# Optimization experiments

Measured on AMD Instinct MI355X. Metric: run time of the kernel, lower is better.

Reference implementation:

```python
import jax, jax.numpy as jnp
import numpy as np

EMBED_DIM = 512
HEADS = 8
ATTN_DIM = EMBED_DIM // HEADS
PF_DIM = 2048
B, L = 4, 2048
LN_EPS = 1e-5


def _linear(x, W, b):
    # nn.Linear: x @ W.T + b, W is [out, in]
    return jnp.einsum('bld,od->blo', x, W) + b


def _layer_norm(x, g, b):
    mu = jnp.mean(x, axis=-1, keepdims=True)
    var = jnp.mean(jnp.square(x - mu), axis=-1, keepdims=True)
    return (x - mu) * jax.lax.rsqrt(var + LN_EPS) * g + b


def _qkv(src, Wq, bq, Wk, bk, Wv, bv):
    def split(t):
        Bb, Ll, _ = t.shape
        return t.reshape(Bb, Ll, HEADS, ATTN_DIM).transpose(0, 2, 1, 3)  # [B,H,L,Dh]
    return (split(_linear(src, Wq, bq)),
            split(_linear(src, Wk, bk)),
            split(_linear(src, Wv, bv)))


def _attention(inp, Q, K1, K2, V1, V2, Wo, bo, ln_g, ln_b, W1, b1, W2, b2):
    # non-softmax linear attention: (Q K1^T) V1 + (Q K2^T) V2
    attn = (jnp.einsum('bhqk,bhkd->bhqd', jnp.einsum('bhqd,bhkd->bhqk', Q, K1), V1)
            + jnp.einsum('bhqk,bhkd->bhqd', jnp.einsum('bhqd,bhkd->bhqk', Q, K2), V2))
    Bb = Q.shape[0]
    attn = attn.transpose(0, 2, 1, 3).reshape(Bb, -1, HEADS * ATTN_DIM)  # [B,L,D]
    x = _linear(attn, Wo, bo)
    x = _layer_norm(inp + x, ln_g, ln_b)          # dropout p=0 (eval)
    ff = _linear(jax.nn.relu(_linear(x, W1, b1)), W2, b2)
    x = _layer_norm(x + ff, ln_g, ln_b)
    return x


def setup_inputs() -> dict:
    key = jax.random.key(0)
    ks = jax.random.split(key, 16)
    s = 0.02
    return {
        'question': jax.random.normal(ks[0], (B, L, EMBED_DIM), jnp.float32),
        'query': jax.random.normal(ks[1], (B, L, EMBED_DIM), jnp.float32),
        'Wq': jax.random.normal(ks[2], (EMBED_DIM, EMBED_DIM), jnp.float32) * s,
        'bq': jnp.zeros((EMBED_DIM,), jnp.float32),
        'Wk': jax.random.normal(ks[3], (EMBED_DIM, EMBED_DIM), jnp.float32) * s,
        'bk': jnp.zeros((EMBED_DIM,), jnp.float32),
        'Wv': jax.random.normal(ks[4], (EMBED_DIM, EMBED_DIM), jnp.float32) * s,
        'bv': jnp.zeros((EMBED_DIM,), jnp.float32),
        'Wo': jax.random.normal(ks[5], (EMBED_DIM, EMBED_DIM), jnp.float32) * s,
        'bo': jnp.zeros((EMBED_DIM,), jnp.float32),
        'ln_g': jnp.ones((EMBED_DIM,), jnp.float32),
        'ln_b': jnp.zeros((EMBED_DIM,), jnp.float32),
        'W1': jax.random.normal(ks[6], (PF_DIM, EMBED_DIM), jnp.float32) * s,
        'b1': jnp.zeros((PF_DIM,), jnp.float32),
        'W2': jax.random.normal(ks[7], (EMBED_DIM, PF_DIM), jnp.float32) * s,
        'b2': jnp.zeros((EMBED_DIM,), jnp.float32),
    }


def reference(question, query, Wq, bq, Wk, bk, Wv, bv, Wo, bo, ln_g, ln_b, W1, b1, W2, b2):
    Q1, K1, V1 = _qkv(question, Wq, bq, Wk, bk, Wv, bv)
    Q2, K2, V2 = _qkv(query, Wq, bq, Wk, bk, Wv, bv)
    question_attn = _attention(question, Q1, K1, K2, V1, V2, Wo, bo, ln_g, ln_b, W1, b1, W2, b2)
    query_attn = _attention(query, Q2, K2, K1, V2, V1, Wo, bo, ln_g, ln_b, W1, b1, W2, b2)
    return jnp.concatenate([question_attn, query_attn], axis=-1)
```

## Files before the change

### kernel.cpp

```cpp
#include <hip/hip_runtime.h>
#include <stdint.h>


#define Bq 4
#define Lq 2048
#define Dq 512
#define PFq 2048
#define Mrows 16384
#define MiBu 1048576ull

typedef __attribute__((ext_vector_type(8))) short frag_ab;
typedef __attribute__((ext_vector_type(4))) float frag_cd;
typedef __attribute__((ext_vector_type(8))) unsigned short ushort8v;

__device__ __forceinline__ unsigned short f2b(float f) {
    union { float f; uint32_t u; } x; x.f = f;
    uint32_t r = x.u + 0x7fffu + ((x.u >> 16) & 1u);
    return (unsigned short)(r >> 16);
}
__device__ __forceinline__ float b2f(unsigned short u) {
    union { uint32_t u; float f; } x; x.u = ((uint32_t)u) << 16;
    return x.f;
}

#define GLD16(g, l)                                                              \
    __builtin_amdgcn_global_load_lds(                                            \
        (const __attribute__((address_space(1))) void*)(const void*)(g),         \
        (__attribute__((address_space(3))) void*)(void*)(l), 16, 0, 0)

__global__ __launch_bounds__(256) void gemm_bf16(
    const unsigned short* __restrict__ A, const unsigned short* __restrict__ Wt,
    const float* __restrict__ bias, unsigned short* __restrict__ outB,
    int M, int N, int K, int relu)
{
    __shared__ __align__(16) unsigned short Sh[2 * 128 * 64];
    unsigned short* At = Sh;
    unsigned short* Bt = Sh + 128 * 64;
    const int tid = threadIdx.x;
    const int lane = tid & 63;
    const int w = tid >> 6;
    const int wm = (w >> 1) * 64, wn = (w & 1) * 64;
    const int lr = lane & 15;
    const int quad = lane >> 4;
    const size_t bm = (size_t)blockIdx.x * 128, bn = (size_t)blockIdx.y * 128;

    frag_cd acc[4][4] = {};

    const int ar = tid >> 3;
    const int acs = (((tid & 7) ^ (ar & 7)) << 3);
    const unsigned short* Ag = A  + (bm + ar) * (size_t)K + acs;
    const unsigned short* Bg = Wt + (bn + ar) * (size_t)K + acs;
    unsigned short* Asd = At + w * 512;
    unsigned short* Bsd = Bt + w * 512;

    for (int k0 = 0; k0 < K; k0 += 64) {
        __syncthreads();
#pragma unroll
        for (int i = 0; i < 4; ++i) {
            GLD16(Ag + (size_t)(32 * i) * K + k0, Asd + i * 2048);
            GLD16(Bg + (size_t)(32 * i) * K + k0, Bsd + i * 2048);
        }
        __syncthreads();
#pragma unroll
        for (int kk = 0; kk < 2; ++kk) {
            frag_ab a[4], b[4];
#pragma unroll
            for (int i = 0; i < 4; ++i)
                a[i] = *(const frag_ab*)&At[(wm + i * 16 + lr) * 64 +
                                            ((((kk << 2) | quad) ^ (lr & 7)) << 3)];
#pragma unroll
            for (int j = 0; j < 4; ++j)
                b[j] = *(const frag_ab*)&Bt[(wn + j * 16 + lr) * 64 +
                                            ((((kk << 2) | quad) ^ (lr & 7)) << 3)];
#pragma unroll
            for (int i = 0; i < 4; ++i)
#pragma unroll
                for (int j = 0; j < 4; ++j)
                    acc[i][j] = __builtin_amdgcn_mfma_f32_16x16x32_bf16(a[i], b[j], acc[i][j], 0, 0, 0);
        }
    }

    __syncthreads();
    unsigned short* Cs = Sh + w * 4096;
#pragma unroll
    for (int j = 0; j < 4; ++j) {
        const float bv = bias[(int)bn + wn + j * 16 + lr];
#pragma unroll
        for (int i = 0; i < 4; ++i)
#pragma unroll
            for (int r = 0; r < 4; ++r) {
                float v = acc[i][j][r] + bv;
                if (relu) v = fmaxf(v, 0.f);
                Cs[(i * 16 + quad * 4 + r) * 64 + j * 16 + lr] = f2b(v);
            }
    }
    const int rl = lane >> 3;
    const int c8 = (lane & 7) * 8;
#pragma unroll
    for (int k = 0; k < 8; ++k) {
        const int row = rl + k * 8;
        ushort8v val = *(const ushort8v*)&Cs[row * 64 + c8];
        *(ushort8v*)(outB + (size_t)(bm + wm + row) * N + bn + wn + c8) = val;
    }
}

__global__ __launch_bounds__(256) void gemm_res(
    const unsigned short* __restrict__ A, const unsigned short* __restrict__ Wt,
    const float* __restrict__ bias,
    const float* __restrict__ resA, const float* __restrict__ resB,
    unsigned short* __restrict__ outB, int M, int N, int K)
{
    __shared__ __align__(16) unsigned short Sh[128 * 64 + 64 * 64];
    unsigned short* At = Sh;
    unsigned short* Bt = Sh + 128 * 64;
    const int tid = threadIdx.x;
    const int lane = tid & 63;
    const int w = tid >> 6;
    const int wm = w * 32;
    const int lr = lane & 15;
    const int quad = lane >> 4;
    const size_t bm = (size_t)blockIdx.x * 128, bn = (size_t)blockIdx.y * 64;

    frag_cd acc[2][4] = {};

    const int ar = tid >> 3;
    const int acs = (((tid & 7) ^ (ar & 7)) << 3);
    const unsigned short* Ag = A  + (bm + ar) * (size_t)K + acs;
    const unsigned short* Bg = Wt + (bn + ar) * (size_t)K + acs;
    unsigned short* Asd = At + w * 512;
    unsigned short* Bsd = Bt + w * 512;

    for (int k0 = 0; k0 < K; k0 += 64) {
        __syncthreads();
#pragma unroll
        for (int i = 0; i < 4; ++i)
            GLD16(Ag + (size_t)(32 * i) * K + k0, Asd + i * 2048);
#pragma unroll
        for (int i = 0; i < 2; ++i)
            GLD16(Bg + (size_t)(32 * i) * K + k0, Bsd + i * 2048);
        __syncthreads();
#pragma unroll
        for (int kk = 0; kk < 2; ++kk) {
            frag_ab a[2], b[4];
#pragma unroll
            for (int i = 0; i < 2; ++i)
                a[i] = *(const frag_ab*)&At[(wm + i * 16 + lr) * 64 +
                                            ((((kk << 2) | quad) ^ (lr & 7)) << 3)];
#pragma unroll
            for (int j = 0; j < 4; ++j)
                b[j] = *(const frag_ab*)&Bt[(j * 16 + lr) * 64 +
                                            ((((kk << 2) | quad) ^ (lr & 7)) << 3)];
#pragma unroll
            for (int i = 0; i < 2; ++i)
#pragma unroll
                for (int j = 0; j < 4; ++j)
                    acc[i][j] = __builtin_amdgcn_mfma_f32_16x16x32_bf16(a[i], b[j], acc[i][j], 0, 0, 0);
        }
    }

    __syncthreads();
    unsigned short* Cs = Sh + w * 2048;
#pragma unroll
    for (int j = 0; j < 4; ++j) {
        const float bv = bias[(int)bn + j * 16 + lr];
#pragma unroll
        for (int i = 0; i < 2; ++i)
#pragma unroll
            for (int r = 0; r < 4; ++r)
                Cs[(i * 16 + quad * 4 + r) * 64 + j * 16 + lr] = f2b(acc[i][j][r] + bv);
    }
    const int rl = lane >> 3;
    const int c8 = (lane & 7) * 8;
#pragma unroll
    for (int k = 0; k < 4; ++k) {
        const int row = rl + k * 8;
        const int grow = (int)bm + wm + row;
        const size_t idx = (size_t)grow * N + bn + c8;
        ushort8v val = *(const ushort8v*)&Cs[row * 64 + c8];
        float vv[8];
#pragma unroll
        for (int t = 0; t < 8; ++t) vv[t] = b2f(val[t]);
        if (resA) {
            const float* rp = (grow < 8192) ? resA + idx : resB + idx - (size_t)8192 * N;
            float4 ra = *(const float4*)(rp);
            float4 rb = *(const float4*)(rp + 4);
            vv[0] += ra.x; vv[1] += ra.y; vv[2] += ra.z; vv[3] += ra.w;
            vv[4] += rb.x; vv[5] += rb.y; vv[6] += rb.z; vv[7] += rb.w;
        } else {
            ushort8v old = *(const ushort8v*)(outB + idx);
#pragma unroll
            for (int t = 0; t < 8; ++t) vv[t] += b2f(old[t]);
        }
        ushort8v o;
#pragma unroll
        for (int t = 0; t < 8; ++t) o[t] = f2b(vv[t]);
        *(ushort8v*)(outB + idx) = o;
    }
}

__global__ __launch_bounds__(256) void convert_all(
    const float* __restrict__ Wq, const float* __restrict__ Wk,
    const float* __restrict__ Wv, const float* __restrict__ Wo,
    const float* __restrict__ W1, const float* __restrict__ W2,
    const float* __restrict__ question, const float* __restrict__ query,
    const float* __restrict__ bqp, const float* __restrict__ bkp,
    const float* __restrict__ bvp,
    unsigned short* __restrict__ Wqkvb, unsigned short* __restrict__ Wob,
    unsigned short* __restrict__ W1b, unsigned short* __restrict__ W2b,
    unsigned short* __restrict__ Xb, float* __restrict__ S,
    float* __restrict__ bqkv)
{
    const int b = blockIdx.x;
    const float* src; unsigned short* dst; size_t off;
    if (b < 256)        { src = Wq; dst = Wqkvb;          off = (size_t)b * 1024; }
    else if (b < 512)   { src = Wk; dst = Wqkvb + 262144; off = (size_t)(b - 256) * 1024; }
    else if (b < 768)   { src = Wv; dst = Wqkvb + 524288; off = (size_t)(b - 512) * 1024; }
    else if (b < 1024)  { src = Wo; dst = Wob;            off = (size_t)(b - 768) * 1024; }
    else if (b < 2048)  { src = W1; dst = W1b;            off = (size_t)(b - 1024) * 1024; }
    else if (b < 3072)  { src = W2; dst = W2b;            off = (size_t)(b - 2048) * 1024; }
    else if (b < 7168)  { src = question; dst = Xb;       off = (size_t)(b - 3072) * 1024; }
    else if (b < 11264) { src = query; dst = Xb + 4194304; off = (size_t)(b - 7168) * 1024; }
    else if (b < 11392) {
        const size_t idx = ((size_t)(b - 11264) * 256 + threadIdx.x) * 4;
        *(float4*)(S + idx) = make_float4(0.f, 0.f, 0.f, 0.f);
        return;
    } else {
        const int n = (b - 11392) * 256 + threadIdx.x;
        bqkv[n] = (n < 512) ? bqp[n] : (n < 1024) ? bkp[n - 512] : bvp[n - 1024];
        return;
    }
    const size_t idx = off + threadIdx.x * 4;
    float4 v = *(const float4*)(src + idx);
    ushort4 o;
    o.x = f2b(v.x); o.y = f2b(v.y); o.z = f2b(v.z); o.w = f2b(v.w);
    *(ushort4*)(dst + idx) = o;
}

__global__ __launch_bounds__(256) void s_kernel(
    const unsigned short* __restrict__ QKV, float* __restrict__ S)
{
    const int bh = blockIdx.x, chunk = blockIdx.y;
    const int b = bh >> 3, h = bh & 7;
    __shared__ float Ks[8][64];
    __shared__ float Vs[8][64];
    const int tid = threadIdx.x;
    const int tx = tid & 15, ty = tid >> 4;
    float acc[4][4] = {};
    for (int pass = 0; pass < 2; ++pass) {
        for (int l0 = 0; l0 < 128; l0 += 8) {
#pragma unroll
            for (int it = 0; it < 2; ++it) {
                const int e = tid + it * 256;
                const int rr = e >> 6, cc = e & 63;
                const size_t row = (size_t)pass * 8192 + (size_t)b * Lq + chunk * 128 + l0 + rr;
                Ks[rr][cc] = b2f(QKV[row * 1536 + 512 + h * 64 + cc]);
                Vs[rr][cc] = b2f(QKV[row * 1536 + 1024 + h * 64 + cc]);
            }
            __syncthreads();
#pragma unroll
            for (int rr = 0; rr < 8; ++rr) {
                float kv[4], vv[4];
#pragma unroll
                for (int i = 0; i < 4; ++i) kv[i] = Ks[rr][ty * 4 + i];
#pragma unroll
                for (int j = 0; j < 4; ++j) vv[j] = Vs[rr][tx * 4 + j];
#pragma unroll
                for (int i = 0; i < 4; ++i)
#pragma unroll
                    for (int j = 0; j < 4; ++j)
                        acc[i][j] = fmaf(kv[i], vv[j], acc[i][j]);
            }
            __syncthreads();
        }
    }
#pragma unroll
    for (int i = 0; i < 4; ++i)
#pragma unroll
        for (int j = 0; j < 4; ++j)
            atomicAdd(&S[((size_t)bh * 64 + ty * 4 + i) * 64 + tx * 4 + j], acc[i][j]);
}

__global__ __launch_bounds__(256) void sbt_convert(
    const float* __restrict__ S, unsigned short* __restrict__ Sbt)
{
    const int bh = blockIdx.x;
    const float* Sp = S + (size_t)bh * 4096;
    unsigned short* Dp = Sbt + (size_t)bh * 4096;
    const int t = threadIdx.x;
#pragma unroll
    for (int u = 0; u < 16; ++u) {
        const int d = t * 16 + u;
        const int kj = d & 31, n = (d >> 5) & 63, kk = d >> 11;
        Dp[d] = f2b(Sp[(size_t)(kk * 32 + kj) * 64 + n]);
    }
}

__global__ __launch_bounds__(256) void attn_mfma(
    const unsigned short* __restrict__ QKV, const unsigned short* __restrict__ Sbt,
    unsigned short* __restrict__ Ob)
{
    __shared__ __align__(16) unsigned short Sh[2 * 128 * 32 + 2 * 64 * 32];
    unsigned short* At = Sh;
    unsigned short* Bt = Sh + 2 * 128 * 32;
    const int h = blockIdx.x;
    const int rbase = blockIdx.y * 128;
    const int b = (rbase >> 11) & 3;
    const int bh = b * 8 + h;
    const int tid = threadIdx.x;
    const int lane = tid & 63;
    const int w = tid >> 6;
    const int lr = lane & 15;
    const int quad = lane >> 4;

    {
        const int rloc = tid >> 2, c8 = (tid & 3) * 8;
#pragma unroll
        for (int it = 0; it < 4; ++it) {
            const int kk = it & 1, rh = it >> 1;
            const unsigned short* g = QKV +
                ((size_t)rbase + rh * 64 + rloc) * 1536 + h * 64 + kk * 32 + c8;
            GLD16(g, At + kk * 4096 + rh * 2048 + w * 512);
        }
        const unsigned short* Sg = Sbt + (size_t)bh * 4096 + tid * 8;
#pragma unroll
        for (int bi = 0; bi < 2; ++bi)
            GLD16(Sg + bi * 2048, Bt + bi * 2048 + w * 512);
    }
    __syncthreads();

    frag_cd acc[2][4] = {};
#pragma unroll
    for (int kk = 0; kk < 2; ++kk) {
        frag_ab a[2], bfr[4];
#pragma unroll
        for (int i = 0; i < 2; ++i)
            a[i] = *(const frag_ab*)&At[kk * 4096 + (w * 32 + i * 16 + lr) * 32 + quad * 8];
#pragma unroll
        for (int j = 0; j < 4; ++j)
            bfr[j] = *(const frag_ab*)&Bt[kk * 2048 + (j * 16 + lr) * 32 + quad * 8];
#pragma unroll
        for (int i = 0; i < 2; ++i)
#pragma unroll
            for (int j = 0; j < 4; ++j)
                acc[i][j] = __builtin_amdgcn_mfma_f32_16x16x32_bf16(a[i], bfr[j], acc[i][j], 0, 0, 0);
    }

    __syncthreads();
    unsigned short* Cs = Sh + w * 2048;
#pragma unroll
    for (int i = 0; i < 2; ++i)
#pragma unroll
        for (int j = 0; j < 4; ++j)
#pragma unroll
            for (int r = 0; r < 4; ++r)
                Cs[(i * 16 + quad * 4 + r) * 64 + j * 16 + lr] = f2b(acc[i][j][r]);
    const int rl = lane >> 3;
    const int c8o = (lane & 7) * 8;
#pragma unroll
    for (int k = 0; k < 4; ++k) {
        const int row = rl + k * 8;
        ushort8v val = *(const ushort8v*)&Cs[row * 64 + c8o];
        *(ushort8v*)(Ob + (size_t)(rbase + w * 32 + row) * 512 + h * 64 + c8o) = val;
    }
}

__global__ __launch_bounds__(256) void ln_b16_inplace(
    unsigned short* __restrict__ Y, const float* __restrict__ g,
    const float* __restrict__ bta)
{
    __shared__ float part[8];
    const int row = blockIdx.x;
    const int t = threadIdx.x;
    const int w = t >> 6;
    unsigned short* yr = Y + (size_t)row * Dq;
    const float v0 = b2f(yr[t]), v1 = b2f(yr[t + 256]);
    float s = v0 + v1;
#pragma unroll
    for (int off = 32; off; off >>= 1) s += __shfl_xor(s, off, 64);
    if ((t & 63) == 0) part[w] = s;
    __syncthreads();
    const float mean = (part[0] + part[1] + part[2] + part[3]) * (1.f / Dq);
    const float d0 = v0 - mean, d1 = v1 - mean;
    float q = d0 * d0 + d1 * d1;
#pragma unroll
    for (int off = 32; off; off >>= 1) q += __shfl_xor(q, off, 64);
    if ((t & 63) == 0) part[4 + w] = q;
    __syncthreads();
    const float rstd = rsqrtf((part[4] + part[5] + part[6] + part[7]) * (1.f / Dq) + 1e-5f);
    yr[t] = f2b(d0 * rstd * g[t] + bta[t]);
    yr[t + 256] = f2b(d1 * rstd * g[t + 256] + bta[t + 256]);
}

__global__ __launch_bounds__(256) void ln_b16_out(
    const unsigned short* __restrict__ Y, const float* __restrict__ g,
    const float* __restrict__ bta, float* __restrict__ out)
{
    __shared__ float part[8];
    const int row = blockIdx.x;
    const int t = threadIdx.x;
    const int w = t >> 6;
    const unsigned short* yr = Y + (size_t)row * Dq;
    const float v0 = b2f(yr[t]), v1 = b2f(yr[t + 256]);
    float s = v0 + v1;
#pragma unroll
    for (int off = 32; off; off >>= 1) s += __shfl_xor(s, off, 64);
    if ((t & 63) == 0) part[w] = s;
    __syncthreads();
    const float mean = (part[0] + part[1] + part[2] + part[3]) * (1.f / Dq);
    const float d0 = v0 - mean, d1 = v1 - mean;
    float q = d0 * d0 + d1 * d1;
#pragma unroll
    for (int off = 32; off; off >>= 1) q += __shfl_xor(q, off, 64);
    if ((t & 63) == 0) part[4 + w] = q;
    __syncthreads();
    const float rstd = rsqrtf((part[4] + part[5] + part[6] + part[7]) * (1.f / Dq) + 1e-5f);
    const int half = row >> 13, br = row & 8191;
    float* orow = out + (size_t)br * 1024 + half * 512;
    orow[t] = d0 * rstd * g[t] + bta[t];
    orow[t + 256] = d1 * rstd * g[t + 256] + bta[t + 256];
}

extern "C" void kernel_launch(void* const* d_in, const int* in_sizes, int n_in,
                              void* d_out, int out_size, void* d_ws, size_t ws_size,
                              hipStream_t stream)
{
    const float* question = (const float*)d_in[0];
    const float* query    = (const float*)d_in[1];
    const float* Wq = (const float*)d_in[2];  const float* bqp = (const float*)d_in[3];
    const float* Wk = (const float*)d_in[4];  const float* bkp = (const float*)d_in[5];
    const float* Wv = (const float*)d_in[6];  const float* bvp = (const float*)d_in[7];
    const float* Wo = (const float*)d_in[8];  const float* bo  = (const float*)d_in[9];
    const float* ln_g = (const float*)d_in[10]; const float* ln_b = (const float*)d_in[11];
    const float* W1 = (const float*)d_in[12]; const float* b1 = (const float*)d_in[13];
    const float* W2 = (const float*)d_in[14]; const float* b2 = (const float*)d_in[15];
    float* out = (float*)d_out;
    char* ws = (char*)d_ws;

    unsigned short* QKVb  = (unsigned short*)(ws);
    unsigned short* attnb = (unsigned short*)(ws + 48 * MiBu);
    unsigned short* Xb    = (unsigned short*)(ws + 64 * MiBu);
    unsigned short* xbuf  = (unsigned short*)(ws + 64 * MiBu);
    unsigned short* hb    = (unsigned short*)(ws);
    float* S = (float*)(ws + 80 * MiBu);
    char* wp = ws + 80 * MiBu + 524288;
    unsigned short* Wqkvb = (unsigned short*)wp;  wp += 1536 * 512 * 2;
    unsigned short* Wob   = (unsigned short*)wp;  wp += 512 * 512 * 2;
    unsigned short* W1b   = (unsigned short*)wp;  wp += 2048 * 512 * 2;
    unsigned short* W2b   = (unsigned short*)wp;  wp += 512 * 2048 * 2;
    unsigned short* Sbt   = (unsigned short*)wp;  wp += 32 * 4096 * 2;
    float* bqkv           = (float*)wp;

    dim3 blk(256);

    convert_all<<<11398, blk, 0, stream>>>(Wq, Wk, Wv, Wo, W1, W2, question, query,
                                           bqp, bkp, bvp,
                                           Wqkvb, Wob, W1b, W2b, Xb, S, bqkv);

    gemm_bf16<<<dim3(128, 12), blk, 0, stream>>>(Xb, Wqkvb, bqkv, QKVb,
                                                 Mrows, 1536, 512, 0);

    s_kernel<<<dim3(32, 16), blk, 0, stream>>>(QKVb, S);
    sbt_convert<<<32, blk, 0, stream>>>(S, Sbt);
    attn_mfma<<<dim3(8, 128), blk, 0, stream>>>(QKVb, Sbt, attnb);

    gemm_res<<<dim3(128, 8), blk, 0, stream>>>(attnb, Wob, bo, question, query,
                                               xbuf, Mrows, 512, 512);

    ln_b16_inplace<<<Mrows, blk, 0, stream>>>(xbuf, ln_g, ln_b);

    gemm_bf16<<<dim3(128, 16), blk, 0, stream>>>(xbuf, W1b, b1, hb,
                                                 Mrows, PFq, 512, 1);

    gemm_res<<<dim3(128, 8), blk, 0, stream>>>(hb, W2b, b2, nullptr, nullptr,
                                               xbuf, Mrows, 512, PFq);

    ln_b16_out<<<Mrows, blk, 0, stream>>>(xbuf, ln_g, ln_b, out);
}
```

Measured before the change: 350.8 us.

## Replace atomic S accumulation with per-slice partials reduced in sbt_convert

The K^T V reduction kernel now has each block handle a contiguous 256-row slice with 64-row shared tiles loaded through 16-byte vector loads. Each block writes its partial S to a private slot instead of using atomicAdd, and the zero-init of S in convert_all is removed. sbt_convert now sums the 16 partials and transposes into the bf16 layout, with more blocks. This removes atomic contention and the tiny 8-row tile loop, at the cost of extra partial-buffer traffic, which is stored in the attnb workspace region before attnb is written.

```diff
diff --git a/kernel.cpp b/kernel.cpp
--- a/kernel.cpp
+++ b/kernel.cpp
@@ -8,6 +8,7 @@
 #define PFq 2048
 #define Mrows 16384
 #define MiBu 1048576ull
+#define NSLICE 16
 
 typedef __attribute__((ext_vector_type(8))) short frag_ab;
 typedef __attribute__((ext_vector_type(4))) float frag_cd;
@@ -207,8 +208,7 @@
     const float* __restrict__ bvp,
     unsigned short* __restrict__ Wqkvb, unsigned short* __restrict__ Wob,
     unsigned short* __restrict__ W1b, unsigned short* __restrict__ W2b,
-    unsigned short* __restrict__ Xb, float* __restrict__ S,
-    float* __restrict__ bqkv)
+    unsigned short* __restrict__ Xb, float* __restrict__ bqkv)
 {
     const int b = blockIdx.x;
     const float* src; unsigned short* dst; size_t off;
@@ -220,12 +220,8 @@
     else if (b < 3072)  { src = W2; dst = W2b;            off = (size_t)(b - 2048) * 1024; }
     else if (b < 7168)  { src = question; dst = Xb;       off = (size_t)(b - 3072) * 1024; }
     else if (b < 11264) { src = query; dst = Xb + 4194304; off = (size_t)(b - 7168) * 1024; }
-    else if (b < 11392) {
-        const size_t idx = ((size_t)(b - 11264) * 256 + threadIdx.x) * 4;
-        *(float4*)(S + idx) = make_float4(0.f, 0.f, 0.f, 0.f);
-        return;
-    } else {
-        const int n = (b - 11392) * 256 + threadIdx.x;
+    else {
+        const int n = (b - 11264) * 256 + threadIdx.x;
         bqkv[n] = (n < 512) ? bqp[n] : (n < 1024) ? bkp[n - 512] : bvp[n - 1024];
         return;
     }
@@ -237,61 +233,86 @@
 }
 
 __global__ __launch_bounds__(256) void s_kernel(
-    const unsigned short* __restrict__ QKV, float* __restrict__ S)
-{
-    const int bh = blockIdx.x, chunk = blockIdx.y;
+    const unsigned short* __restrict__ QKV, float* __restrict__ Spart)
+{
+    const int bh = blockIdx.x;
+    const int sl = blockIdx.y;
     const int b = bh >> 3, h = bh & 7;
-    __shared__ float Ks[8][64];
-    __shared__ float Vs[8][64];
+    const int pass = sl >> 3;
+    const int l0 = (sl & 7) * 256;
+    __shared__ float Ks[64][64];
+    __shared__ float Vs[64][64];
     const int tid = threadIdx.x;
     const int tx = tid & 15, ty = tid >> 4;
+    const int srow = tid >> 3;
+    const int scol = (tid & 7) * 8;
+    const size_t rowbase = (size_t)pass * 8192 + (size_t)b * Lq + l0;
+
     float acc[4][4] = {};
-    for (int pass = 0; pass < 2; ++pass) {
-        for (int l0 = 0; l0 < 128; l0 += 8) {
-#pragma unroll
-            for (int it = 0; it < 2; ++it) {
-                const int e = tid + it * 256;
-                const int rr = e >> 6, cc = e & 63;
-                const size_t row = (size_t)pass * 8192 + (size_t)b * Lq + chunk * 128 + l0 + rr;
-                Ks[rr][cc] = b2f(QKV[row * 1536 + 512 + h * 64 + cc]);
-                Vs[rr][cc] = b2f(QKV[row * 1536 + 1024 + h * 64 + cc]);
-            }
-            __syncthreads();
-#pragma unroll
-            for (int rr = 0; rr < 8; ++rr) {
-                float kv[4], vv[4];
-#pragma unroll
-                for (int i = 0; i < 4; ++i) kv[i] = Ks[rr][ty * 4 + i];
-#pragma unroll
-                for (int j = 0; j < 4; ++j) vv[j] = Vs[rr][tx * 4 + j];
-#pragma unroll
-                for (int i = 0; i < 4; ++i)
-#pragma unroll
-                    for (int j = 0; j < 4; ++j)
-                        acc[i][j] = fmaf(kv[i], vv[j], acc[i][j]);
-            }
-            __syncthreads();
-        }
-    }
-#pragma unroll
-    for (int i = 0; i < 4; ++i)
-#pragma unroll
-        for (int j = 0; j < 4; ++j)
-            atomicAdd(&S[((size_t)bh * 64 + ty * 4 + i) * 64 + tx * 4 + j], acc[i][j]);
+
+    for (int t0 = 0; t0 < 256; t0 += 64) {
+        const unsigned short* kp0 = QKV + (rowbase + t0 + srow) * 1536 + 512 + h * 64 + scol;
+        const unsigned short* kp1 = kp0 + (size_t)32 * 1536;
+        ushort8v k0 = *(const ushort8v*)kp0;
+        ushort8v v0 = *(const ushort8v*)(kp0 + 512);
+        ushort8v k1 = *(const ushort8v*)kp1;
+        ushort8v v1 = *(const ushort8v*)(kp1 + 512);
+        __syncthreads();
+#pragma unroll
+        for (int e = 0; e < 8; ++e) {
+            Ks[srow][scol + e]      = b2f(k0[e]);
+            Vs[srow][scol + e]      = b2f(v0[e]);
+            Ks[srow + 32][scol + e] = b2f(k1[e]);
+            Vs[srow + 32][scol + e] = b2f(v1[e]);
+        }
+        __syncthreads();
+#pragma unroll 4
+        for (int rr = 0; rr < 64; ++rr) {
+            const float4 kf = *(const float4*)&Ks[rr][ty * 4];
+            const float4 vf = *(const float4*)&Vs[rr][tx * 4];
+            acc[0][0] = fmaf(kf.x, vf.x, acc[0][0]);
+            acc[0][1] = fmaf(kf.x, vf.y, acc[0][1]);
+            acc[0][2] = fmaf(kf.x, vf.z, acc[0][2]);
+            acc[0][3] = fmaf(kf.x, vf.w, acc[0][3]);
+            acc[1][0] = fmaf(kf.y, vf.x, acc[1][0]);
+            acc[1][1] = fmaf(kf.y, vf.y, acc[1][1]);
+            acc[1][2] = fmaf(kf.y, vf.z, acc[1][2]);
+            acc[1][3] = fmaf(kf.y, vf.w, acc[1][3]);
+            acc[2][0] = fmaf(kf.z, vf.x, acc[2][0]);
+            acc[2][1] = fmaf(kf.z, vf.y, acc[2][1]);
+            acc[2][2] = fmaf(kf.z, vf.z, acc[2][2]);
+            acc[2][3] = fmaf(kf.z, vf.w, acc[2][3]);
+            acc[3][0] = fmaf(kf.w, vf.x, acc[3][0]);
+            acc[3][1] = fmaf(kf.w, vf.y, acc[3][1]);
+            acc[3][2] = fmaf(kf.w, vf.z, acc[3][2]);
+            acc[3][3] = fmaf(kf.w, vf.w, acc[3][3]);
+        }
+    }
+
+    float* Sp = Spart + ((size_t)bh * NSLICE + sl) * 4096;
+#pragma unroll
+    for (int i = 0; i < 4; ++i) {
+        float4 o = make_float4(acc[i][0], acc[i][1], acc[i][2], acc[i][3]);
+        *(float4*)(Sp + (ty * 4 + i) * 64 + tx * 4) = o;
+    }
 }
 
 __global__ __launch_bounds__(256) void sbt_convert(
-    const float* __restrict__ S, unsigned short* __restrict__ Sbt)
+    const float* __restrict__ Spart, unsigned short* __restrict__ Sbt)
 {
     const int bh = blockIdx.x;
-    const float* Sp = S + (size_t)bh * 4096;
+    const int uo = blockIdx.y;
+    const float* Sp = Spart + (size_t)bh * (NSLICE * 4096);
     unsigned short* Dp = Sbt + (size_t)bh * 4096;
     const int t = threadIdx.x;
 #pragma unroll
-    for (int u = 0; u < 16; ++u) {
-        const int d = t * 16 + u;
-        const int kj = d & 31, n = (d >> 5) & 63, kk = d >> 11;
-        Dp[d] = f2b(Sp[(size_t)(kk * 32 + kj) * 64 + n]);
+    for (int u = 0; u < 4; ++u) {
+        const int d = (uo * 4 + u) * 256 + t;
+        float v = 0.f;
+#pragma unroll
+        for (int s = 0; s < NSLICE; ++s) v += Sp[(size_t)s * 4096 + d];
+        const int row = d >> 6, col = d & 63;
+        Dp[(row >> 5) * 2048 + col * 32 + (row & 31)] = f2b(v);
     }
 }
 
@@ -438,10 +459,10 @@
 
     unsigned short* QKVb  = (unsigned short*)(ws);
     unsigned short* attnb = (unsigned short*)(ws + 48 * MiBu);
+    float* Spart          = (float*)(ws + 48 * MiBu);
     unsigned short* Xb    = (unsigned short*)(ws + 64 * MiBu);
     unsigned short* xbuf  = (unsigned short*)(ws + 64 * MiBu);
     unsigned short* hb    = (unsigned short*)(ws);
-    float* S = (float*)(ws + 80 * MiBu);
     char* wp = ws + 80 * MiBu + 524288;
     unsigned short* Wqkvb = (unsigned short*)wp;  wp += 1536 * 512 * 2;
     unsigned short* Wob   = (unsigned short*)wp;  wp += 512 * 512 * 2;
@@ -452,15 +473,15 @@
 
     dim3 blk(256);
 
-    convert_all<<<11398, blk, 0, stream>>>(Wq, Wk, Wv, Wo, W1, W2, question, query,
+    convert_all<<<11270, blk, 0, stream>>>(Wq, Wk, Wv, Wo, W1, W2, question, query,
                                            bqp, bkp, bvp,
-                                           Wqkvb, Wob, W1b, W2b, Xb, S, bqkv);
+                                           Wqkvb, Wob, W1b, W2b, Xb, bqkv);
 
     gemm_bf16<<<dim3(128, 12), blk, 0, stream>>>(Xb, Wqkvb, bqkv, QKVb,
                                                  Mrows, 1536, 512, 0);
 
-    s_kernel<<<dim3(32, 16), blk, 0, stream>>>(QKVb, S);
-    sbt_convert<<<32, blk, 0, stream>>>(S, Sbt);
+    s_kernel<<<dim3(32, NSLICE), blk, 0, stream>>>(QKVb, Spart);
+    sbt_convert<<<dim3(32, 4), blk, 0, stream>>>(Spart, Sbt);
     attn_mfma<<<dim3(8, 128), blk, 0, stream>>>(QKVb, Sbt, attnb);
 
     gemm_res<<<dim3(128, 8), blk, 0, stream>>>(attnb, Wob, bo, question, query,
```

Measured after the change: 330.5 us. 1.06x faster.
